# Kernel tuning notes

Hardware: AMD Instinct MI355X
Metric: run time of the kernel (lower is better)

## Reference

```python
import jax, jax.numpy as jnp
import numpy as np

# Dimensions (see shape_source)
B, C, H, W = 8, 3, 256, 256
WIDTH = 32   # FNO width
MODES = 12   # modes1 == modes2
L = 4        # number of FNO layers
GAP = 4      # encoder_de sample_gap
PAD = 9      # trans_net.padding


def _downsample(x):
    # Faithful vectorized form of encoder_de.output: keep indices i % GAP == 0
    # (output size int((N-1)/GAP)+1 == number of multiples of GAP below N).
    return x[:, :, ::GAP, ::GAP]


def _spectral_conv(x, w1, w2):
    # SpectralConv2d: rfft2 -> low-mode complex channel mix -> irfft2
    Hp, Wp = x.shape[-2], x.shape[-1]
    x_ft = jnp.fft.rfft2(x)  # [B, WIDTH, Hp, Wp//2+1] complex64
    out_ft = jnp.zeros((x.shape[0], w1.shape[1], Hp, Wp // 2 + 1), dtype=jnp.complex64)
    out_ft = out_ft.at[:, :, :MODES, :MODES].set(
        jnp.einsum('bixy,ioxy->boxy', x_ft[:, :, :MODES, :MODES], w1))
    out_ft = out_ft.at[:, :, -MODES:, :MODES].set(
        jnp.einsum('bixy,ioxy->boxy', x_ft[:, :, -MODES:, :MODES], w2))
    return jnp.fft.irfft2(out_ft, s=(Hp, Wp))


def _forward(x_en, fc0_w, fc0_b, w1r, w1i, w2r, w2i, pw_w, pw_b,
             fc1_w, fc1_b, fc2_w, fc2_b):
    x_de = _downsample(x_en)
    # fc0 on channels-last, back to channels-first
    x = jnp.einsum('bchw,cd->bdhw', x_en, fc0_w) + fc0_b[None, :, None, None]
    # F.pad(x, [0, PAD, 0, PAD]) pads right/bottom of last two dims
    x = jnp.pad(x, ((0, 0), (0, 0), (0, PAD), (0, PAD)))
    for l in range(L):
        w1 = (w1r[l] + 1j * w1i[l]).astype(jnp.complex64)
        w2 = (w2r[l] + 1j * w2i[l]).astype(jnp.complex64)
        x1 = _spectral_conv(x, w1, w2)
        x2 = jnp.einsum('bihw,oi->bohw', x, pw_w[l]) + pw_b[l][None, :, None, None]
        x = x1 + x2
        if l < L - 1:  # last layer has no activation
            x = jax.nn.gelu(x, approximate=False)  # torch F.gelu default = exact erf
    trans_out = x[..., :-PAD, :-PAD].transpose(0, 2, 3, 1)  # [B,H,W,WIDTH]
    h = jax.nn.gelu(trans_out @ fc1_w + fc1_b, approximate=False)  # [B,H,W,128]
    pred_delta = (h @ fc2_w + fc2_b).transpose(0, 3, 1, 2)          # [B,3,H,W]
    pred = pred_delta + x_en
    pred_de = _downsample(pred)
    return pred_de, x_de, pred, x_en


def setup_inputs() -> dict:
    key = jax.random.key(0)
    ks = jax.random.split(key, 14)
    scale = 1.0 / (WIDTH * WIDTH)
    f32 = jnp.float32
    x_en = jax.random.normal(ks[0], (B, C, H, W), f32)
    ctr = jnp.zeros((B, 1), f32)  # accepted but unused by trans_net.forward
    fc0_w = jax.random.normal(ks[1], (3, WIDTH), f32) * 0.2
    fc0_b = jnp.zeros((WIDTH,), f32)
    # torch.rand(..., dtype=cfloat): uniform [0,1) real and imag parts
    w1r = scale * jax.random.uniform(ks[2], (L, WIDTH, WIDTH, MODES, MODES), f32)
    w1i = scale * jax.random.uniform(ks[3], (L, WIDTH, WIDTH, MODES, MODES), f32)
    w2r = scale * jax.random.uniform(ks[4], (L, WIDTH, WIDTH, MODES, MODES), f32)
    w2i = scale * jax.random.uniform(ks[5], (L, WIDTH, WIDTH, MODES, MODES), f32)
    pw_w = jax.random.normal(ks[6], (L, WIDTH, WIDTH), f32) / np.sqrt(WIDTH)  # 1x1 conv [out,in]
    pw_b = jnp.zeros((L, WIDTH), f32)
    fc1_w = jax.random.normal(ks[7], (WIDTH, 128), f32) / np.sqrt(WIDTH)
    fc1_b = jnp.zeros((128,), f32)
    fc2_w = jax.random.normal(ks[8], (128, 3), f32) / np.sqrt(128.0)
    fc2_b = jnp.zeros((3,), f32)
    return dict(x_en=x_en, ctr=ctr, fc0_w=fc0_w, fc0_b=fc0_b,
                w1r=w1r, w1i=w1i, w2r=w2r, w2i=w2i,
                pw_w=pw_w, pw_b=pw_b, fc1_w=fc1_w, fc1_b=fc1_b,
                fc2_w=fc2_w, fc2_b=fc2_b)


def reference(x_en, ctr, fc0_w, fc0_b, w1r, w1i, w2r, w2i, pw_w, pw_b,
              fc1_w, fc1_b, fc2_w, fc2_b):
    del ctr  # unused in the original trans_net.forward
    return _forward(x_en, fc0_w, fc0_b, w1r, w1i, w2r, w2i, pw_w, pw_b,
                    fc1_w, fc1_b, fc2_w, fc2_b)
```

## Files before the change

### kernel.cpp

```cpp
#include <hip/hip_runtime.h>
#include <math.h>

#define HP 265
#define NPIX 70225
#define ROWF 8480
#define TWO_PI 6.28318530717958647692f

#define OFF_X     0
#define OFF_U     8988800
#define OFF_G     10752640
#define OFF_A     11342464
#define OFF_TFB   12427904
#define OFF_TS    12432512
#define OFF_W1B   12436864
#define OFF_W2B   12438912
#define OFF_PWB   12439936

typedef __attribute__((ext_vector_type(8))) short short8;
typedef __attribute__((ext_vector_type(4))) float f32x4;

__device__ __forceinline__ float gelu_f(float v){
  float x2 = v*v;
  float p  = fmaf(x2, 0.10295597f, 2.30212056f);
  float tn = -v*p;
  float e  = __builtin_amdgcn_exp2f(tn);
  float r  = __builtin_amdgcn_rcpf(1.0f + e);
  return v * r;
}
__device__ __forceinline__ unsigned short f2b(float f){
  unsigned u = __float_as_uint(f);
  u += 0x7FFFu + ((u >> 16) & 1u);
  return (unsigned short)(u >> 16);
}
__device__ __forceinline__ unsigned cvtpk(float lo, float hi){
  unsigned r;
  asm("v_cvt_pk_bf16_f32 %0, %1, %2" : "=v"(r) : "v"(lo), "v"(hi));
  return r;
}
__device__ __forceinline__ short8 mk8(unsigned a, unsigned b, unsigned c, unsigned d){
  union { uint4 u; short8 s; } t;
  t.u = make_uint4(a, b, c, d);
  return t.s;
}

__device__ __forceinline__ void init_body(int idx,
                       unsigned short* __restrict__ Tfb, unsigned short* __restrict__ Ts,
                       unsigned short* __restrict__ w1b, unsigned short* __restrict__ w2b,
                       unsigned short* __restrict__ pwb,
                       const float* __restrict__ fc1w, const float* __restrict__ fc2w,
                       const float* __restrict__ pw_w){
  if (idx < 32*288){
    int m = idx / 288, hc = idx % 288;
    unsigned short v = 0;
    if (m < 26 && hc < 265){
      int k = m >> 1;
      int t = (hc*k) % HP;
      float s, c; sincosf(TWO_PI*(float)t/(float)HP, &s, &c);
      v = f2b((m & 1) ? -s : c);
    }
    Tfb[idx] = v;
  }
  if (idx < 272*32){
    int w = idx >> 5, kap = idx & 31;
    unsigned short v = 0;
    if (w < HP && kap < 24){
      int k = kap >> 1;
      int t = (w*k) % HP;
      float s, c; sincosf(TWO_PI*(float)t/(float)HP, &s, &c);
      const float invN = 1.f/70225.f;
      float val = (!(kap&1)) ? invN*(k==0 ? 1.f : 2.f*c)
                             : ((k==0) ? 0.f : -invN*2.f*s);
      v = f2b(val);
    }
    Ts[idx] = v;
  }
  if (idx < 4096){
    int n = idx >> 5, s = idx & 31;
    int gg = s >> 3, q = s & 7;
    int ch = (q < 4) ? (gg*4 + q) : (16 + gg*4 + (q - 4));
    w1b[idx] = f2b(fc1w[ch*128 + n]);
  }
  if (idx < 2048){
    int n = idx >> 7, k = idx & 127;
    w2b[idx] = (n < 3) ? f2b(fc2w[k*3 + n]) : (unsigned short)0;
  }
  if (idx < 4096)
    pwb[idx] = f2b(pw_w[idx]);
}

__global__ __launch_bounds__(256) void k_fc0(const float* __restrict__ xen,
                                             const float* __restrict__ w0,
                                             const float* __restrict__ b0,
                                             unsigned short* __restrict__ xb,
                                             float* __restrict__ out,
                                             unsigned short* __restrict__ Tfb,
                                             unsigned short* __restrict__ Ts,
                                             unsigned short* __restrict__ w1b,
                                             unsigned short* __restrict__ w2b,
                                             unsigned short* __restrict__ pwb,
                                             const float* __restrict__ fc1w,
                                             const float* __restrict__ fc2w,
                                             const float* __restrict__ pw_w){
  if (blockIdx.x >= 2195){
    init_body((blockIdx.x - 2195)*256 + threadIdx.x, Tfb, Ts, w1b, w2b, pwb,
              fc1w, fc2w, pw_w);
    return;
  }
  int idx = blockIdx.x*256 + threadIdx.x;
  if (idx >= 8*NPIX) return;
  int w = idx % HP; int t = idx / HP; int h = t % HP; int b = t / HP;
  float o32[32];
  if (h < 256 && w < 256){
    const float* xp = xen + (((size_t)b*3)*256 + h)*256 + w;
    float c0 = xp[0], c1 = xp[65536], c2 = xp[131072];
    #pragma unroll
    for (int d = 0; d < 32; ++d)
      o32[d] = b0[d] + c0*w0[d] + c1*w0[32+d] + c2*w0[64+d];
    size_t be = ((size_t)b*3)*65536 + (h<<8) + w;
    out[1769472 + be]          = c0;
    out[1769472 + be + 65536]  = c1;
    out[1769472 + be + 131072] = c2;
    if (((h|w)&3) == 0){
      size_t db = ((size_t)b*3)*4096 + ((h>>2)<<6) + (w>>2);
      out[98304 + db]        = c0;
      out[98304 + db + 4096] = c1;
      out[98304 + db + 8192] = c2;
    }
  } else {
    #pragma unroll
    for (int d = 0; d < 32; ++d) o32[d] = 0.f;
  }
  uint4* dst = (uint4*)(xb + (size_t)idx*32);
  #pragma unroll
  for (int q = 0; q < 4; ++q)
    dst[q] = make_uint4(cvtpk(o32[8*q],o32[8*q+1]),   cvtpk(o32[8*q+2],o32[8*q+3]),
                        cvtpk(o32[8*q+4],o32[8*q+5]), cvtpk(o32[8*q+6],o32[8*q+7]));
}

__global__ __launch_bounds__(256) void k_dftm(const unsigned short* __restrict__ xb,
                                              const unsigned short* __restrict__ Tfb,
                                              float* __restrict__ U32){
  int tid = threadIdx.x;
  int wv = tid>>6, lane = tid&63, lr = lane&15, g = lane>>4, lk = g*8;
  int n0 = blockIdx.x*64;
  int b  = blockIdx.y;
  int n  = n0 + wv*16 + lr;
  const unsigned short* xcol = xb + (size_t)b*HP*ROWF + n;
  f32x4 acc0 = {0.f,0.f,0.f,0.f}, acc1 = {0.f,0.f,0.f,0.f};
  #pragma unroll
  for (int kc = 0; kc < 9; ++kc){
    short8 hv;
    int hb = kc*32 + lk;
    #pragma unroll
    for (int q = 0; q < 8; ++q){
      int h = hb + q;
      hv[q] = (h < HP) ? (short)xcol[(size_t)h*ROWF] : (short)0;
    }
    short8 aT0 = *(const short8*)&Tfb[lr*288 + kc*32 + lk];
    short8 aT1 = *(const short8*)&Tfb[(16+lr)*288 + kc*32 + lk];
    acc0 = __builtin_amdgcn_mfma_f32_16x16x32_bf16(aT0, hv, acc0, 0,0,0);
    acc1 = __builtin_amdgcn_mfma_f32_16x16x32_bf16(aT1, hv, acc1, 0,0,0);
  }
  if (n < 8480){
    #pragma unroll
    for (int r = 0; r < 4; ++r){
      int m0 = g*4 + r;
      U32[((size_t)b*26 + m0)*8480 + n] = acc0[r];
      int m1 = 16 + m0;
      if (m1 < 26) U32[((size_t)b*26 + m1)*8480 + n] = acc1[r];
    }
  }
}

__global__ __launch_bounds__(256) void k_spec(const float* __restrict__ U32,
                                              const float* __restrict__ w1r,
                                              const float* __restrict__ w1i,
                                              const float* __restrict__ w2r,
                                              const float* __restrict__ w2i,
                                              float2* __restrict__ G, int l){
  __shared__ float part[256*25];
  __shared__ float Xs[32*25];
  int j = blockIdx.x;
  int b = blockIdx.y;
  int ws = blockIdx.z;
  int tid = threadIdx.x;
  int wsub = tid >> 5, i = tid & 31;
  int kk   = (j < 12) ? j : (24 - j);
  bool cj  = (j >= 12);
  float xr[12], xi[12];
  #pragma unroll
  for (int k = 0; k < 12; ++k){ xr[k] = 0.f; xi[k] = 0.f; }
  const float* ubr = U32 + ((size_t)(b*26 + 2*kk))*8480;
  for (int w = ws*8 + wsub; w < HP; w += 32){
    int n = w*32 + i;
    float ux = ubr[n];
    float uy = ubr[8480 + n];
    if (cj) uy = -uy;
    float bs, bc; sincosf(-TWO_PI*(float)w/(float)HP, &bs, &bc);
    float pr = 1.f, pi = 0.f;
    #pragma unroll
    for (int k = 0; k < 12; ++k){
      xr[k] = fmaf(ux, pr, fmaf(-uy, pi, xr[k]));
      xi[k] = fmaf(ux, pi, fmaf( uy, pr, xi[k]));
      float npr = pr*bc - pi*bs;
      pi = fmaf(pr, bs, pi*bc);
      pr = npr;
    }
  }
  #pragma unroll
  for (int k = 0; k < 12; ++k){
    part[tid*25 + 2*k]     = xr[k];
    part[tid*25 + 2*k + 1] = xi[k];
  }
  __syncthreads();
  {
    int sg = tid >> 5;
    int ii = tid & 31;
    #pragma unroll
    for (int s0 = 0; s0 < 3; ++s0){
      int s = sg*3 + s0;
      float acc = 0.f;
      #pragma unroll
      for (int wq = 0; wq < 8; ++wq) acc += part[(wq*32 + ii)*25 + s];
      Xs[ii*25 + s] = acc;
    }
  }
  __syncthreads();
  int ky = (j < 12) ? j : (j - 12);
  const float* wr = (j < 12) ? w1r : w2r;
  const float* wi = (j < 12) ? w1i : w2i;
  float2* Gp = G + (size_t)ws*73728;
  for (int p = tid; p < 384; p += 256){
    int o = p / 12, kx = p % 12;
    size_t wbase = (size_t)l*147456 + (size_t)o*144 + (size_t)ky*12 + kx;
    float gr = 0.f, gi = 0.f;
    #pragma unroll 4
    for (int i2 = 0; i2 < 32; ++i2){
      float xvr = Xs[i2*25 + 2*kx];
      float xvi = Xs[i2*25 + 2*kx + 1];
      float a = wr[wbase + (size_t)i2*4608];
      float c = wi[wbase + (size_t)i2*4608];
      gr += xvr*a - xvi*c;
      gi += xvr*c + xvi*a;
    }
    Gp[((size_t)(b*32 + o)*24 + j)*12 + kx] = make_float2(gr, gi);
  }
}

__global__ __launch_bounds__(320) void k_idft_h(const float2* __restrict__ G,
                                                unsigned short* __restrict__ A16){
  __shared__ float2 gs[288];
  int bo = blockIdx.x;
  for (int i = threadIdx.x; i < 288; i += 320){
    float2 g0 = G[(size_t)bo*288 + i];
    float2 g1 = G[73728 + (size_t)bo*288 + i];
    float2 g2 = G[2*73728 + (size_t)bo*288 + i];
    float2 g3 = G[3*73728 + (size_t)bo*288 + i];
    gs[i] = make_float2(g0.x+g1.x+g2.x+g3.x, g0.y+g1.y+g2.y+g3.y);
  }
  __syncthreads();
  if (threadIdx.x >= 133) return;
  int h = blockIdx.y*133 + threadIdx.x;
  if (h >= HP) return;
  float ar[12], ai[12];
  #pragma unroll
  for (int k = 0; k < 12; ++k){ ar[k] = 0.f; ai[k] = 0.f; }
  for (int j = 0; j < 24; ++j){
    int ky = (j < 12) ? j : (241 + j);
    int t = (ky*h) % HP;
    float s, c; sincosf(TWO_PI*(float)t/(float)HP, &s, &c);
    #pragma unroll
    for (int k = 0; k < 12; ++k){
      float2 g = gs[j*12 + k];
      ar[k] = fmaf(g.x, c, fmaf(-g.y, s, ar[k]));
      ai[k] = fmaf(g.x, s, fmaf( g.y, c, ai[k]));
    }
  }
  int b = bo >> 5, o = bo & 31;
  uint4* ap = (uint4*)(A16 + (((size_t)(b*HP + h))*32 + o)*32);
  #pragma unroll
  for (int q = 0; q < 3; ++q)
    ap[q] = make_uint4(cvtpk(ar[4*q],   ai[4*q]),   cvtpk(ar[4*q+1], ai[4*q+1]),
                       cvtpk(ar[4*q+2], ai[4*q+2]), cvtpk(ar[4*q+3], ai[4*q+3]));
  ap[3] = make_uint4(0u, 0u, 0u, 0u);
}

__global__ __launch_bounds__(256) void k_final(const unsigned short* __restrict__ A16,
                                               const unsigned short* __restrict__ Tsyn,
                                               const unsigned short* __restrict__ pwb,
                                               const float* __restrict__ pw_b,
                                               unsigned short* __restrict__ xb, int l){
  int tid = threadIdx.x;
  int wv = tid>>6, lane = tid&63, lr = lane&15, g = lane>>4, lk = g*8;
  int h = blockIdx.x*4 + wv;
  int b = blockIdx.y;
  int z = blockIdx.z;
  if (h >= HP) return;
  const unsigned short* arow = A16 + (size_t)(b*HP + h)*1024;
  short8 aA0 = *(const short8*)&arow[lr*32 + lk];
  short8 aA1 = *(const short8*)&arow[(16+lr)*32 + lk];
  short8 aP0 = *(const short8*)&pwb[l*1024 + lr*32 + lk];
  short8 aP1 = *(const short8*)&pwb[l*1024 + (16+lr)*32 + lk];
  float4 vb0 = *(const float4*)&pw_b[l*32 + g*4];
  float4 vb1 = *(const float4*)&pw_b[l*32 + 16 + g*4];
  unsigned short* xrow = xb + (size_t)(b*HP + h)*ROWF;
  const f32x4 z4 = {0.f,0.f,0.f,0.f};
  const int wt0 = z ? 9 : 0, wt1 = z ? 17 : 9;
  int w = wt0*16 + lr;
  short8 bT = *(const short8*)&Tsyn[(size_t)w*32 + lk];
  short8 bX = *(const short8*)&xrow[(size_t)w*32 + lk];
  #pragma unroll
  for (int wt = wt0; wt < wt1; ++wt){
    short8 nT, nX;
    if (wt + 1 < wt1){
      int wn = (wt+1)*16 + lr;
      nT = *(const short8*)&Tsyn[(size_t)wn*32 + lk];
      nX = *(const short8*)&xrow[(size_t)wn*32 + lk];
    }
    f32x4 a0 = __builtin_amdgcn_mfma_f32_16x16x32_bf16(aA0, bT, z4, 0,0,0);
    a0 = __builtin_amdgcn_mfma_f32_16x16x32_bf16(aP0, bX, a0, 0,0,0);
    f32x4 a1 = __builtin_amdgcn_mfma_f32_16x16x32_bf16(aA1, bT, z4, 0,0,0);
    a1 = __builtin_amdgcn_mfma_f32_16x16x32_bf16(aP1, bX, a1, 0,0,0);
    if (w < HP){
      float v0[4], v1[4];
      v0[0]=a0[0]+vb0.x; v0[1]=a0[1]+vb0.y; v0[2]=a0[2]+vb0.z; v0[3]=a0[3]+vb0.w;
      v1[0]=a1[0]+vb1.x; v1[1]=a1[1]+vb1.y; v1[2]=a1[2]+vb1.z; v1[3]=a1[3]+vb1.w;
      #pragma unroll
      for (int r = 0; r < 4; ++r){ v0[r] = gelu_f(v0[r]); v1[r] = gelu_f(v1[r]); }
      *(uint2*)&xrow[(size_t)w*32 + g*4] =
          make_uint2(cvtpk(v0[0],v0[1]), cvtpk(v0[2],v0[3]));
      *(uint2*)&xrow[(size_t)w*32 + 16 + g*4] =
          make_uint2(cvtpk(v1[0],v1[1]), cvtpk(v1[2],v1[3]));
    }
    bT = nT; bX = nX; w += 16;
  }
}

__global__ __launch_bounds__(256) void k_last(const unsigned short* __restrict__ A16,
                                              const unsigned short* __restrict__ Tsyn,
                                              const unsigned short* __restrict__ pwb,
                                              const float* __restrict__ pw_b,
                                              const unsigned short* __restrict__ xb,
                                              const float* __restrict__ xen,
                                              const unsigned short* __restrict__ w1bp,
                                              const float* __restrict__ fc1b,
                                              const unsigned short* __restrict__ w2b,
                                              const float* __restrict__ fc2b,
                                              float* __restrict__ out){
  __shared__ unsigned short Pm[4][16*136];
  int tid = threadIdx.x;
  int wv = tid>>6, lane = tid&63, lr = lane&15, g = lane>>4, lk = g*8;
  int h = blockIdx.x*4 + wv;
  int b = blockIdx.y;
  int z = blockIdx.z;
  const int l = 3;
  const unsigned short* arow = A16 + (size_t)(b*HP + h)*1024;
  short8 aA0 = *(const short8*)&arow[lr*32 + lk];
  short8 aA1 = *(const short8*)&arow[(16+lr)*32 + lk];
  short8 aP0 = *(const short8*)&pwb[l*1024 + lr*32 + lk];
  short8 aP1 = *(const short8*)&pwb[l*1024 + (16+lr)*32 + lk];
  float4 vb0 = *(const float4*)&pw_b[l*32 + g*4];
  float4 vb1 = *(const float4*)&pw_b[l*32 + 16 + g*4];
  short8 bf1[8], bf2[4];
  #pragma unroll
  for (int nt = 0; nt < 8; ++nt)
    bf1[nt] = *(const short8*)&w1bp[(nt*16+lr)*32 + lk];
  #pragma unroll
  for (int ks = 0; ks < 4; ++ks)
    bf2[ks] = *(const short8*)&w2b[lr*128 + ks*32 + lk];
  float f2c = (lr < 3) ? fc2b[lr] : 0.f;
  const unsigned short* xrow = xb + (size_t)(b*HP + h)*ROWF;
  unsigned short* P = Pm[wv];
  const f32x4 z4 = {0.f,0.f,0.f,0.f};
  for (int wt = z*8; wt < z*8 + 8; ++wt){
    int w0 = wt*16;
    int w = w0 + lr;
    short8 bT = *(const short8*)&Tsyn[(size_t)w*32 + lk];
    short8 bX = *(const short8*)&xrow[(size_t)w*32 + lk];
    f32x4 a0 = __builtin_amdgcn_mfma_f32_16x16x32_bf16(aA0, bT, z4, 0,0,0);
    a0 = __builtin_amdgcn_mfma_f32_16x16x32_bf16(aP0, bX, a0, 0,0,0);
    f32x4 a1 = __builtin_amdgcn_mfma_f32_16x16x32_bf16(aA1, bT, z4, 0,0,0);
    a1 = __builtin_amdgcn_mfma_f32_16x16x32_bf16(aP1, bX, a1, 0,0,0);
    float v0[4], v1[4];
    v0[0]=a0[0]+vb0.x; v0[1]=a0[1]+vb0.y; v0[2]=a0[2]+vb0.z; v0[3]=a0[3]+vb0.w;
    v1[0]=a1[0]+vb1.x; v1[1]=a1[1]+vb1.y; v1[2]=a1[2]+vb1.z; v1[3]=a1[3]+vb1.w;
    short8 xf = mk8(cvtpk(v0[0],v0[1]), cvtpk(v0[2],v0[3]),
                    cvtpk(v1[0],v1[1]), cvtpk(v1[2],v1[3]));
    f32x4 acc[8];
    #pragma unroll
    for (int nt = 0; nt < 8; ++nt)
      acc[nt] = __builtin_amdgcn_mfma_f32_16x16x32_bf16(bf1[nt], xf, z4, 0,0,0);
    #pragma unroll
    for (int nt = 0; nt < 8; ++nt){
      float4 bb = *(const float4*)&fc1b[nt*16 + g*4];
      float h0 = gelu_f(acc[nt][0] + bb.x);
      float h1 = gelu_f(acc[nt][1] + bb.y);
      float h2 = gelu_f(acc[nt][2] + bb.z);
      float h3 = gelu_f(acc[nt][3] + bb.w);
      *(uint2*)&P[lr*136 + nt*16 + g*4] =
          make_uint2(cvtpk(h0,h1), cvtpk(h2,h3));
    }
    f32x4 a2 = z4;
    #pragma unroll
    for (int ks = 0; ks < 4; ++ks){
      short8 ap = *(const short8*)&P[lr*136 + ks*32 + lk];
      a2 = __builtin_amdgcn_mfma_f32_16x16x32_bf16(ap, bf2[ks], a2, 0,0,0);
    }
    if (lr < 3){
      size_t base = ((size_t)(b*3 + lr))*65536 + (h<<8) + w0 + g*4;
      float4 xe = *(const float4*)&xen[base];
      float4 pr;
      pr.x = a2[0] + f2c + xe.x;
      pr.y = a2[1] + f2c + xe.y;
      pr.z = a2[2] + f2c + xe.z;
      pr.w = a2[3] + f2c + xe.w;
      *(float4*)&out[196608 + base] = pr;
      if ((h & 3) == 0){
        int w4 = (w0 + g*4) >> 2;
        out[((size_t)(b*3 + lr))*4096 + ((h>>2)<<6) + w4] = pr.x;
      }
    }
  }
}

extern "C" void kernel_launch(void* const* d_in, const int* in_sizes, int n_in,
                              void* d_out, int out_size, void* d_ws, size_t ws_size,
                              hipStream_t stream){
  const float* x_en  = (const float*)d_in[0];
  const float* fc0_w = (const float*)d_in[2];
  const float* fc0_b = (const float*)d_in[3];
  const float* w1r   = (const float*)d_in[4];
  const float* w1i   = (const float*)d_in[5];
  const float* w2r   = (const float*)d_in[6];
  const float* w2i   = (const float*)d_in[7];
  const float* pw_w  = (const float*)d_in[8];
  const float* pw_b  = (const float*)d_in[9];
  const float* fc1_w = (const float*)d_in[10];
  const float* fc1_b = (const float*)d_in[11];
  const float* fc2_w = (const float*)d_in[12];
  const float* fc2_b = (const float*)d_in[13];
  float* out = (float*)d_out;
  float* ws  = (float*)d_ws;

  unsigned short* xb  = (unsigned short*)(ws + OFF_X);
  float*  U32         = ws + OFF_U;
  float2* G           = (float2*)(ws + OFF_G);
  unsigned short* A16 = (unsigned short*)(ws + OFF_A);
  unsigned short* Tfb = (unsigned short*)(ws + OFF_TFB);
  unsigned short* Ts  = (unsigned short*)(ws + OFF_TS);
  unsigned short* w1b = (unsigned short*)(ws + OFF_W1B);
  unsigned short* w2b = (unsigned short*)(ws + OFF_W2B);
  unsigned short* pwb = (unsigned short*)(ws + OFF_PWB);

  k_fc0<<<2231, 256, 0, stream>>>(x_en, fc0_w, fc0_b, xb, out,
                                  Tfb, Ts, w1b, w2b, pwb, fc1_w, fc2_w, pw_w);
  for (int l = 0; l < 4; ++l){
    k_dftm<<<dim3(133,8), 256, 0, stream>>>(xb, Tfb, U32);
    k_spec<<<dim3(24,8,4), 256, 0, stream>>>(U32, w1r, w1i, w2r, w2i, G, l);
    k_idft_h<<<dim3(256,2), 320, 0, stream>>>(G, A16);
    if (l < 3)
      k_final<<<dim3(67,8,2), 256, 0, stream>>>(A16, Ts, pwb, pw_b, xb, l);
  }
  k_last<<<dim3(64,8,2), 256, 0, stream>>>(A16, Ts, pwb, pw_b, xb, x_en,
                                           w1b, fc1_b, w2b, fc2_b, out);
}
```

Baseline: 282.1 us.

## Split DFT, spectral, inverse-DFT and final kernels across more blocks

The H-direction DFT is split into two halves over a new grid z dimension. Each half writes its own U slab, and k_spec sums the two slabs when it reads them. k_spec uses 8 w-stride partitions instead of 4, k_idft_h splits H into 4 chunks, and k_final and k_last split W into 4 tiles. The goal is more blocks per launch to fill the GPU's compute units. The cost is extra partial-sum traffic and reduction work.

```diff
diff --git a/kernel.cpp b/kernel.cpp
--- a/kernel.cpp
+++ b/kernel.cpp
@@ -5,16 +5,19 @@
 #define NPIX 70225
 #define ROWF 8480
 #define TWO_PI 6.28318530717958647692f
+#define USLAB 1763840
+#define GSLAB 73728
 
 #define OFF_X     0
 #define OFF_U     8988800
-#define OFF_G     10752640
-#define OFF_A     11342464
-#define OFF_TFB   12427904
-#define OFF_TS    12432512
-#define OFF_W1B   12436864
-#define OFF_W2B   12438912
-#define OFF_PWB   12439936
+#define OFF_G     12516480
+#define OFF_A     13696128
+#define OFF_TFB   14781568
+#define OFF_TFB1  14786176
+#define OFF_TS    14788736
+#define OFF_W1B   14793088
+#define OFF_W2B   14795136
+#define OFF_PWB   14796160
 
 typedef __attribute__((ext_vector_type(8))) short short8;
 typedef __attribute__((ext_vector_type(4))) float f32x4;
@@ -44,7 +47,8 @@
 }
 
 __device__ __forceinline__ void init_body(int idx,
-                       unsigned short* __restrict__ Tfb, unsigned short* __restrict__ Ts,
+                       unsigned short* __restrict__ Tfb, unsigned short* __restrict__ Tfb1,
+                       unsigned short* __restrict__ Ts,
                        unsigned short* __restrict__ w1b, unsigned short* __restrict__ w2b,
                        unsigned short* __restrict__ pwb,
                        const float* __restrict__ fc1w, const float* __restrict__ fc2w,
@@ -60,6 +64,18 @@
     }
     Tfb[idx] = v;
   }
+  if (idx < 32*160){
+    int m = idx / 160, hc = idx % 160;
+    int habs = 133 + hc;
+    unsigned short v = 0;
+    if (m < 26 && habs < 265){
+      int k = m >> 1;
+      int t = (habs*k) % HP;
+      float s, c; sincosf(TWO_PI*(float)t/(float)HP, &s, &c);
+      v = f2b((m & 1) ? -s : c);
+    }
+    Tfb1[idx] = v;
+  }
   if (idx < 272*32){
     int w = idx >> 5, kap = idx & 31;
     unsigned short v = 0;
@@ -94,6 +110,7 @@
                                              unsigned short* __restrict__ xb,
                                              float* __restrict__ out,
                                              unsigned short* __restrict__ Tfb,
+                                             unsigned short* __restrict__ Tfb1,
                                              unsigned short* __restrict__ Ts,
                                              unsigned short* __restrict__ w1b,
                                              unsigned short* __restrict__ w2b,
@@ -102,7 +119,7 @@
                                              const float* __restrict__ fc2w,
                                              const float* __restrict__ pw_w){
   if (blockIdx.x >= 2195){
-    init_body((blockIdx.x - 2195)*256 + threadIdx.x, Tfb, Ts, w1b, w2b, pwb,
+    init_body((blockIdx.x - 2195)*256 + threadIdx.x, Tfb, Tfb1, Ts, w1b, w2b, pwb,
               fc1w, fc2w, pw_w);
     return;
   }
@@ -139,35 +156,42 @@
 
 __global__ __launch_bounds__(256) void k_dftm(const unsigned short* __restrict__ xb,
                                               const unsigned short* __restrict__ Tfb,
+                                              const unsigned short* __restrict__ Tfb1,
                                               float* __restrict__ U32){
   int tid = threadIdx.x;
   int wv = tid>>6, lane = tid&63, lr = lane&15, g = lane>>4, lk = g*8;
   int n0 = blockIdx.x*64;
   int b  = blockIdx.y;
+  int z  = blockIdx.z;
   int n  = n0 + wv*16 + lr;
+  const int h0   = z ? 133 : 0;
+  const int hcap = z ? 265 : 133;
+  const unsigned short* T = z ? Tfb1 : Tfb;
+  const int trow = z ? 160 : 288;
   const unsigned short* xcol = xb + (size_t)b*HP*ROWF + n;
   f32x4 acc0 = {0.f,0.f,0.f,0.f}, acc1 = {0.f,0.f,0.f,0.f};
   #pragma unroll
-  for (int kc = 0; kc < 9; ++kc){
+  for (int kc = 0; kc < 5; ++kc){
     short8 hv;
-    int hb = kc*32 + lk;
+    int hb = h0 + kc*32 + lk;
     #pragma unroll
     for (int q = 0; q < 8; ++q){
       int h = hb + q;
-      hv[q] = (h < HP) ? (short)xcol[(size_t)h*ROWF] : (short)0;
-    }
-    short8 aT0 = *(const short8*)&Tfb[lr*288 + kc*32 + lk];
-    short8 aT1 = *(const short8*)&Tfb[(16+lr)*288 + kc*32 + lk];
+      hv[q] = (h < hcap) ? (short)xcol[(size_t)h*ROWF] : (short)0;
+    }
+    short8 aT0 = *(const short8*)&T[lr*trow + kc*32 + lk];
+    short8 aT1 = *(const short8*)&T[(16+lr)*trow + kc*32 + lk];
     acc0 = __builtin_amdgcn_mfma_f32_16x16x32_bf16(aT0, hv, acc0, 0,0,0);
     acc1 = __builtin_amdgcn_mfma_f32_16x16x32_bf16(aT1, hv, acc1, 0,0,0);
   }
   if (n < 8480){
+    float* Uz = U32 + (size_t)z*USLAB;
     #pragma unroll
     for (int r = 0; r < 4; ++r){
       int m0 = g*4 + r;
-      U32[((size_t)b*26 + m0)*8480 + n] = acc0[r];
+      Uz[((size_t)b*26 + m0)*8480 + n] = acc0[r];
       int m1 = 16 + m0;
-      if (m1 < 26) U32[((size_t)b*26 + m1)*8480 + n] = acc1[r];
+      if (m1 < 26) Uz[((size_t)b*26 + m1)*8480 + n] = acc1[r];
     }
   }
 }
@@ -191,10 +215,10 @@
   #pragma unroll
   for (int k = 0; k < 12; ++k){ xr[k] = 0.f; xi[k] = 0.f; }
   const float* ubr = U32 + ((size_t)(b*26 + 2*kk))*8480;
-  for (int w = ws*8 + wsub; w < HP; w += 32){
+  for (int w = ws*8 + wsub; w < HP; w += 64){
     int n = w*32 + i;
-    float ux = ubr[n];
-    float uy = ubr[8480 + n];
+    float ux = ubr[n]        + ubr[USLAB + n];
+    float uy = ubr[8480 + n] + ubr[USLAB + 8480 + n];
     if (cj) uy = -uy;
     float bs, bc; sincosf(-TWO_PI*(float)w/(float)HP, &bs, &bc);
     float pr = 1.f, pi = 0.f;
@@ -229,7 +253,7 @@
   int ky = (j < 12) ? j : (j - 12);
   const float* wr = (j < 12) ? w1r : w2r;
   const float* wi = (j < 12) ? w1i : w2i;
-  float2* Gp = G + (size_t)ws*73728;
+  float2* Gp = G + (size_t)ws*GSLAB;
   for (int p = tid; p < 384; p += 256){
     int o = p / 12, kx = p % 12;
     size_t wbase = (size_t)l*147456 + (size_t)o*144 + (size_t)ky*12 + kx;
@@ -252,15 +276,17 @@
   __shared__ float2 gs[288];
   int bo = blockIdx.x;
   for (int i = threadIdx.x; i < 288; i += 320){
-    float2 g0 = G[(size_t)bo*288 + i];
-    float2 g1 = G[73728 + (size_t)bo*288 + i];
-    float2 g2 = G[2*73728 + (size_t)bo*288 + i];
-    float2 g3 = G[3*73728 + (size_t)bo*288 + i];
-    gs[i] = make_float2(g0.x+g1.x+g2.x+g3.x, g0.y+g1.y+g2.y+g3.y);
+    float sx = 0.f, sy = 0.f;
+    #pragma unroll
+    for (int p = 0; p < 8; ++p){
+      float2 gp = G[(size_t)p*GSLAB + (size_t)bo*288 + i];
+      sx += gp.x; sy += gp.y;
+    }
+    gs[i] = make_float2(sx, sy);
   }
   __syncthreads();
-  if (threadIdx.x >= 133) return;
-  int h = blockIdx.y*133 + threadIdx.x;
+  if (threadIdx.x >= 67) return;
+  int h = blockIdx.y*67 + threadIdx.x;
   if (h >= HP) return;
   float ar[12], ai[12];
   #pragma unroll
@@ -305,7 +331,8 @@
   float4 vb1 = *(const float4*)&pw_b[l*32 + 16 + g*4];
   unsigned short* xrow = xb + (size_t)(b*HP + h)*ROWF;
   const f32x4 z4 = {0.f,0.f,0.f,0.f};
-  const int wt0 = z ? 9 : 0, wt1 = z ? 17 : 9;
+  const int wt0 = z ? (4*z + 1) : 0;
+  const int wt1 = 4*z + 5;
   int w = wt0*16 + lr;
   short8 bT = *(const short8*)&Tsyn[(size_t)w*32 + lk];
   short8 bX = *(const short8*)&xrow[(size_t)w*32 + lk];
@@ -372,7 +399,7 @@
   const unsigned short* xrow = xb + (size_t)(b*HP + h)*ROWF;
   unsigned short* P = Pm[wv];
   const f32x4 z4 = {0.f,0.f,0.f,0.f};
-  for (int wt = z*8; wt < z*8 + 8; ++wt){
+  for (int wt = z*4; wt < z*4 + 4; ++wt){
     int w0 = wt*16;
     int w = w0 + lr;
     short8 bT = *(const short8*)&Tsyn[(size_t)w*32 + lk];
@@ -442,25 +469,27 @@
   float* out = (float*)d_out;
   float* ws  = (float*)d_ws;
 
-  unsigned short* xb  = (unsigned short*)(ws + OFF_X);
-  float*  U32         = ws + OFF_U;
-  float2* G           = (float2*)(ws + OFF_G);
-  unsigned short* A16 = (unsigned short*)(ws + OFF_A);
-  unsigned short* Tfb = (unsigned short*)(ws + OFF_TFB);
-  unsigned short* Ts  = (unsigned short*)(ws + OFF_TS);
-  unsigned short* w1b = (unsigned short*)(ws + OFF_W1B);
-  unsigned short* w2b = (unsigned short*)(ws + OFF_W2B);
-  unsigned short* pwb = (unsigned short*)(ws + OFF_PWB);
+  unsigned short* xb   = (unsigned short*)(ws + OFF_X);
+  float*  U32          = ws + OFF_U;
+  float2* G            = (float2*)(ws + OFF_G);
+  unsigned short* A16  = (unsigned short*)(ws + OFF_A);
+  unsigned short* Tfb  = (unsigned short*)(ws + OFF_TFB);
+  unsigned short* Tfb1 = (unsigned short*)(ws + OFF_TFB1);
+  unsigned short* Ts   = (unsigned short*)(ws + OFF_TS);
+  unsigned short* w1b  = (unsigned short*)(ws + OFF_W1B);
+  unsigned short* w2b  = (unsigned short*)(ws + OFF_W2B);
+  unsigned short* pwb  = (unsigned short*)(ws + OFF_PWB);
 
   k_fc0<<<2231, 256, 0, stream>>>(x_en, fc0_w, fc0_b, xb, out,
-                                  Tfb, Ts, w1b, w2b, pwb, fc1_w, fc2_w, pw_w);
+                                  Tfb, Tfb1, Ts, w1b, w2b, pwb,
+                                  fc1_w, fc2_w, pw_w);
   for (int l = 0; l < 4; ++l){
-    k_dftm<<<dim3(133,8), 256, 0, stream>>>(xb, Tfb, U32);
-    k_spec<<<dim3(24,8,4), 256, 0, stream>>>(U32, w1r, w1i, w2r, w2i, G, l);
-    k_idft_h<<<dim3(256,2), 320, 0, stream>>>(G, A16);
+    k_dftm<<<dim3(133,8,2), 256, 0, stream>>>(xb, Tfb, Tfb1, U32);
+    k_spec<<<dim3(24,8,8), 256, 0, stream>>>(U32, w1r, w1i, w2r, w2i, G, l);
+    k_idft_h<<<dim3(256,4), 320, 0, stream>>>(G, A16);
     if (l < 3)
-      k_final<<<dim3(67,8,2), 256, 0, stream>>>(A16, Ts, pwb, pw_b, xb, l);
-  }
-  k_last<<<dim3(64,8,2), 256, 0, stream>>>(A16, Ts, pwb, pw_b, xb, x_en,
+      k_final<<<dim3(67,8,4), 256, 0, stream>>>(A16, Ts, pwb, pw_b, xb, l);
+  }
+  k_last<<<dim3(64,8,4), 256, 0, stream>>>(A16, Ts, pwb, pw_b, xb, x_en,
                                            w1b, fc1_b, w2b, fc2_b, out);
 }
```

After: 333.7 us. 18.3% more time.
